# Performance work log

Hardware: AMD Instinct MI355X
Metric: run time of the kernel (lower is better)

The kernel has to match this reference:

```python
import jax, jax.numpy as jnp
import numpy as np

B, N, C = 2, 3072, 768
H = 12                      # num_heads
HD = C // H                 # 64
D = HD // 2                 # 32, rope dim per axis
GRID_H, GRID_W = 48, 64     # 768/16, 1024/16 ; GRID_H*GRID_W == N
BASE = 100.0
EPS = 1e-5


def _rope_tables():
    # positions per token (row-major cartesian product of y,x)
    pos_y = np.repeat(np.arange(GRID_H), GRID_W)   # [N]
    pos_x = np.tile(np.arange(GRID_W), GRID_H)     # [N]
    seq_len = max(GRID_H, GRID_W)
    inv_freq = 1.0 / BASE ** (np.arange(0, D, 2, dtype=np.float32) / D)  # [D/2]
    t = np.arange(seq_len, dtype=np.float32)
    freqs = np.einsum('i,j->ij', t, inv_freq)            # [S, D/2]
    emb = np.concatenate([freqs, freqs], axis=-1)        # [S, D]
    cos, sin = np.cos(emb), np.sin(emb)
    # gather per-token, add head broadcast dims -> [1, 1, N, D]
    mk = lambda tbl, idx: jnp.asarray(tbl[idx][None, None], dtype=jnp.float32)
    return mk(cos, pos_x), mk(sin, pos_x), mk(cos, pos_y), mk(sin, pos_y)


def setup_inputs() -> dict:
    key = jax.random.key(0)
    ks = jax.random.split(key, 12)
    s = 0.02
    cos_x, sin_x, cos_y, sin_y = _rope_tables()
    return {
        'x': jax.random.normal(ks[0], (B, N, C), jnp.float32),
        'w_qkv': jax.random.normal(ks[1], (3 * C, C), jnp.float32) * s,
        'w_proj': jax.random.normal(ks[2], (C, C), jnp.float32) * s,
        'b_proj': jnp.zeros((C,), jnp.float32),
        'g1': jnp.ones((C,), jnp.float32),
        'beta1': jnp.zeros((C,), jnp.float32),
        'g2': jnp.ones((C,), jnp.float32),
        'beta2': jnp.zeros((C,), jnp.float32),
        'w_fc1': jax.random.normal(ks[3], (4 * C, C), jnp.float32) * s,
        'b_fc1': jnp.zeros((4 * C,), jnp.float32),
        'w_fc2': jax.random.normal(ks[4], (C, 4 * C), jnp.float32) * s,
        'b_fc2': jnp.zeros((C,), jnp.float32),
        'cos_x': cos_x, 'sin_x': sin_x, 'cos_y': cos_y, 'sin_y': sin_y,
    }


def _layernorm(x, g, b):
    m = x.mean(-1, keepdims=True)
    v = ((x - m) ** 2).mean(-1, keepdims=True)
    return (x - m) * jax.lax.rsqrt(v + EPS) * g + b


def _rope1d(tok, cos, sin):
    t1, t2 = jnp.split(tok, 2, axis=-1)
    rot = jnp.concatenate([-t2, t1], axis=-1)
    return tok * cos + rot * sin


def _rope2d(tok, cos_x, sin_x, cos_y, sin_y):
    # tok: [B, H, N, HD]; first half of HD is y-coords, second half x-coords
    ty, tx = jnp.split(tok, 2, axis=-1)
    return jnp.concatenate([_rope1d(ty, cos_y, sin_y), _rope1d(tx, cos_x, sin_x)], axis=-1)


def reference(x, w_qkv, w_proj, b_proj, g1, beta1, g2, beta2,
              w_fc1, b_fc1, w_fc2, b_fc2, cos_x, sin_x, cos_y, sin_y):
    # --- attention branch ---
    xn = _layernorm(x, g1, beta1)
    qkv = jnp.einsum('bnc,dc->bnd', xn, w_qkv)           # [B, N, 3C]
    qkv = qkv.reshape(B, N, 3, H, HD).transpose(0, 3, 2, 1, 4)  # [B, H, 3, N, HD]
    q, k, v = qkv[:, :, 0], qkv[:, :, 1], qkv[:, :, 2]
    q = _rope2d(q, cos_x, sin_x, cos_y, sin_y)
    k = _rope2d(k, cos_x, sin_x, cos_y, sin_y)
    scale = HD ** -0.5
    attn = jnp.einsum('bhqd,bhkd->bhqk', q, k) * scale   # [B, H, N, N]
    attn = jax.nn.softmax(attn, axis=-1)
    o = jnp.einsum('bhqk,bhkd->bhqd', attn, v)           # [B, H, N, HD]
    o = o.transpose(0, 2, 1, 3).reshape(B, N, C)
    o = jnp.einsum('bnc,dc->bnd', o, w_proj) + b_proj
    x = x + o
    # --- mlp branch ---
    xn = _layernorm(x, g2, beta2)
    h = jnp.einsum('bnc,hc->bnh', xn, w_fc1) + b_fc1
    h = jax.nn.gelu(h, approximate=False)                # torch nn.GELU default (erf)
    h = jnp.einsum('bnh,ch->bnc', h, w_fc2) + b_fc2
    return x + h
```

## Files before the change

kernel.cpp:

```cpp
#include <hip/hip_runtime.h>
#include <hip/hip_bf16.h>


#define Nn 3072
#define Cc 768
#define Hh 12
#define Mm 6144

typedef unsigned short ushort_t;
typedef unsigned int u32;
using s8v = __attribute__((ext_vector_type(8))) short;
using f4v = __attribute__((ext_vector_type(4))) float;

__device__ __forceinline__ ushort_t f2b(float x){
  u32 u = __float_as_uint(x);
  return (ushort_t)((u + 0x7fffu + ((u >> 16) & 1u)) >> 16);
}
__device__ __forceinline__ u32 pack2(float a, float b){
  return (u32)f2b(a) | ((u32)f2b(b) << 16);
}
__device__ __forceinline__ float b2f(ushort_t u){
  return __uint_as_float(((u32)u) << 16);
}

#define GLD16(g, l) __builtin_amdgcn_global_load_lds( \
    (const __attribute__((address_space(1))) u32*)(g), \
    (__attribute__((address_space(3))) u32*)(l), 16, 0, 0)

__global__ __launch_bounds__(256) void cvt4_kernel(
    const float* __restrict__ a, ushort_t* __restrict__ oa, int na,
    const float* __restrict__ b, ushort_t* __restrict__ ob, int nb,
    const float* __restrict__ c, ushort_t* __restrict__ oc, int nc,
    const float* __restrict__ d, ushort_t* __restrict__ od)
{
  int i = (blockIdx.x*256 + threadIdx.x)*4;
  const float* src; ushort_t* dst;
  if (i < na)           { src = a + i;            dst = oa + i; }
  else if (i < na+nb)   { src = b + (i-na);       dst = ob + (i-na); }
  else if (i < na+nb+nc){ src = c + (i-na-nb);    dst = oc + (i-na-nb); }
  else                  { src = d + (i-na-nb-nc); dst = od + (i-na-nb-nc); }
  float4 v = *(const float4*)src;
  uint2 p; p.x = pack2(v.x, v.y); p.y = pack2(v.z, v.w);
  *(uint2*)dst = p;
}

__global__ __launch_bounds__(256) void ln_kernel(const float* __restrict__ in,
    const float* __restrict__ g, const float* __restrict__ be, ushort_t* __restrict__ out)
{
  int row = blockIdx.x;
  int tid = threadIdx.x;
  size_t base = (size_t)row * Cc;
  float v[3];
  #pragma unroll
  for (int i = 0; i < 3; ++i) v[i] = in[base + tid + i*256];
  __shared__ float red[8];
  float s = v[0]+v[1]+v[2];
  #pragma unroll
  for (int off=32; off; off>>=1) s += __shfl_xor(s, off);
  int wid = tid >> 6, lane = tid & 63;
  if (lane==0) red[wid] = s;
  __syncthreads();
  float mean = (red[0]+red[1]+red[2]+red[3]) * (1.f/Cc);
  float d = 0.f;
  #pragma unroll
  for (int i=0;i<3;++i){ float t = v[i]-mean; d += t*t; }
  #pragma unroll
  for (int off=32; off; off>>=1) d += __shfl_xor(d, off);
  if (lane==0) red[4+wid] = d;
  __syncthreads();
  float var  = (red[4]+red[5]+red[6]+red[7]) * (1.f/Cc);
  float rstd = rsqrtf(var + 1e-5f);
  #pragma unroll
  for (int i=0;i<3;++i){
    int idx = tid + i*256;
    out[base+idx] = f2b((v[i]-mean)*rstd*g[idx] + be[idx]);
  }
}

template<int EPI>
__global__ __launch_bounds__(256) void mgemm_kernel(
    const ushort_t* __restrict__ A, const ushort_t* __restrict__ W,
    const float* __restrict__ bias, const float* __restrict__ residf,
    void* __restrict__ outv, int Nd, int K)
{
  __shared__ __align__(16) ushort_t As[128*32];
  __shared__ __align__(16) ushort_t Ws[128*32];
  int tid = threadIdx.x;
  int w = tid >> 6, lane = tid & 63;
  int g = lane >> 4, c = lane & 15;
  int wr = w >> 1, wc = w & 1;
  int m0 = blockIdx.y * 128, n0 = blockIdx.x * 128;
  int srow = w*32 + (lane >> 2);
  int schunk = (lane & 3) * 8;
  const ushort_t* Ag = A + (size_t)(m0 + srow)*K + schunk;
  const ushort_t* Wg = W + (size_t)(n0 + srow)*K + schunk;
  ushort_t* Asl = &As[w*1024];
  ushort_t* Wsl = &Ws[w*1024];
  f4v acc[4][4] = {};
  for (int k0 = 0; k0 < K; k0 += 32) {
    __syncthreads();
    GLD16(Ag + k0,        Asl);
    GLD16(Ag + 16*K + k0, Asl + 512);
    GLD16(Wg + k0,        Wsl);
    GLD16(Wg + 16*K + k0, Wsl + 512);
    __syncthreads();
    s8v af[4], wf[4];
    #pragma unroll
    for (int i=0;i<4;++i) af[i] = *(const s8v*)&As[(wr*64 + i*16 + c)*32 + g*8];
    #pragma unroll
    for (int j=0;j<4;++j) wf[j] = *(const s8v*)&Ws[(wc*64 + j*16 + c)*32 + g*8];
    #pragma unroll
    for (int i=0;i<4;++i)
      #pragma unroll
      for (int j=0;j<4;++j)
        acc[i][j] = __builtin_amdgcn_mfma_f32_16x16x32_bf16(af[i], wf[j], acc[i][j], 0,0,0);
  }
  #pragma unroll
  for (int j=0;j<4;++j){
    int col = n0 + wc*64 + j*16 + c;
    float bv = (EPI != 0) ? bias[col] : 0.f;
    #pragma unroll
    for (int i=0;i<4;++i){
      int row0 = m0 + wr*64 + i*16 + g*4;
      #pragma unroll
      for (int r=0;r<4;++r){
        float v = acc[i][j][r];
        size_t off = (size_t)(row0 + r)*Nd + col;
        if (EPI == 0) {
          ((ushort_t*)outv)[off] = f2b(v);
        } else if (EPI == 2) {
          float t = v + bv;
          ((ushort_t*)outv)[off] = f2b(0.5f*t*(1.0f + erff(t*0.70710678118654752f)));
        } else {
          ((float*)outv)[off] = v + bv + residf[off];
        }
      }
    }
  }
}

__global__ __launch_bounds__(256) void repack_kernel(
    const ushort_t* __restrict__ qkv,
    const float* __restrict__ cx, const float* __restrict__ sx,
    const float* __restrict__ cy, const float* __restrict__ sy,
    ushort_t* __restrict__ Qb, ushort_t* __restrict__ Kb, ushort_t* __restrict__ Vt)
{
  __shared__ float Vls[64*68];
  int bh = blockIdx.y;
  int b = bh / Hh, h = bh - b*Hh;
  int n0 = blockIdx.x * 64;
  int tid = threadIdx.x;
  int tt = tid >> 2, cch = tid & 3;
  int n = n0 + tt;
  size_t rowbase = (size_t)(b*Nn + n) * 2304 + h*64;

  int half = cch >> 1, ibase = (cch & 1) * 8;
  int d1 = half*32 + ibase;
  const float* ct  = half ? cx : cy;
  const float* st_ = half ? sx : sy;
  float c1[8], s1[8], c2[8], s2[8];
  #pragma unroll
  for (int j=0;j<8;++j){
    c1[j] = ct[n*32 + ibase + j];       s1[j] = st_[n*32 + ibase + j];
    c2[j] = ct[n*32 + ibase + 16 + j];  s2[j] = st_[n*32 + ibase + 16 + j];
  }
  #pragma unroll
  for (int qk = 0; qk < 2; ++qk){
    const ushort_t* src = qkv + rowbase + qk*768;
    uint4 uv1 = *(const uint4*)(src + d1);
    uint4 uv2 = *(const uint4*)(src + d1 + 16);
    float v1[8], v2[8];
    v1[0]=b2f(uv1.x&0xffff); v1[1]=b2f(uv1.x>>16); v1[2]=b2f(uv1.y&0xffff); v1[3]=b2f(uv1.y>>16);
    v1[4]=b2f(uv1.z&0xffff); v1[5]=b2f(uv1.z>>16); v1[6]=b2f(uv1.w&0xffff); v1[7]=b2f(uv1.w>>16);
    v2[0]=b2f(uv2.x&0xffff); v2[1]=b2f(uv2.x>>16); v2[2]=b2f(uv2.y&0xffff); v2[3]=b2f(uv2.y>>16);
    v2[4]=b2f(uv2.z&0xffff); v2[5]=b2f(uv2.z>>16); v2[6]=b2f(uv2.w&0xffff); v2[7]=b2f(uv2.w>>16);
    float sc = qk ? 1.0f : 0.125f;
    float o1[8], o2[8];
    #pragma unroll
    for (int j=0;j<8;++j){
      o1[j] = (v1[j]*c1[j] - v2[j]*s1[j]) * sc;
      o2[j] = (v2[j]*c2[j] + v1[j]*s2[j]) * sc;
    }
    ushort_t* dst = (qk ? Kb : Qb) + ((size_t)bh*Nn + n)*64;
    uint4 u1, u2;
    u1.x = pack2(o1[0],o1[1]); u1.y = pack2(o1[2],o1[3]);
    u1.z = pack2(o1[4],o1[5]); u1.w = pack2(o1[6],o1[7]);
    u2.x = pack2(o2[0],o2[1]); u2.y = pack2(o2[2],o2[3]);
    u2.z = pack2(o2[4],o2[5]); u2.w = pack2(o2[6],o2[7]);
    *(uint4*)(dst + d1)      = u1;
    *(uint4*)(dst + d1 + 16) = u2;
  }

  {
    const ushort_t* src = qkv + rowbase + 1536 + cch*16;
    uint4 ua = *(const uint4*)(src);
    uint4 ub = *(const uint4*)(src + 8);
    float* lp = &Vls[tt*68 + cch*16];
    lp[0]=b2f(ua.x&0xffff); lp[1]=b2f(ua.x>>16); lp[2]=b2f(ua.y&0xffff); lp[3]=b2f(ua.y>>16);
    lp[4]=b2f(ua.z&0xffff); lp[5]=b2f(ua.z>>16); lp[6]=b2f(ua.w&0xffff); lp[7]=b2f(ua.w>>16);
    lp[8]=b2f(ub.x&0xffff); lp[9]=b2f(ub.x>>16); lp[10]=b2f(ub.y&0xffff); lp[11]=b2f(ub.y>>16);
    lp[12]=b2f(ub.z&0xffff); lp[13]=b2f(ub.z>>16); lp[14]=b2f(ub.w&0xffff); lp[15]=b2f(ub.w>>16);
  }
  __syncthreads();
  {
    int d = tid & 63, quarter = tid >> 6;
    float v[16];
    #pragma unroll
    for (int j=0;j<16;++j) v[j] = Vls[(quarter*16 + j)*68 + d];
    uint4 w0, w1;
    w0.x = pack2(v[0],v[1]);   w0.y = pack2(v[2],v[3]);
    w0.z = pack2(v[4],v[5]);   w0.w = pack2(v[6],v[7]);
    w1.x = pack2(v[8],v[9]);   w1.y = pack2(v[10],v[11]);
    w1.z = pack2(v[12],v[13]); w1.w = pack2(v[14],v[15]);
    ushort_t* dst = Vt + ((size_t)bh*64 + d)*Nn + n0 + quarter*16;
    *(uint4*)(dst)     = w0;
    *(uint4*)(dst + 8) = w1;
  }
}

__global__ __launch_bounds__(256) void fattn_kernel(
    const ushort_t* __restrict__ Qb, const ushort_t* __restrict__ Kb,
    const ushort_t* __restrict__ Vt, ushort_t* __restrict__ ob)
{
  __shared__ ushort_t Ks[64*72];
  __shared__ ushort_t Vts[64*72];
  __shared__ ushort_t Ps[4*16*72];
  int bh = blockIdx.y;
  int q0 = blockIdx.x * 64;
  int tid = threadIdx.x;
  int w = tid >> 6, lane = tid & 63, g = lane >> 4, c = lane & 15;

  const ushort_t* qp = Qb + ((size_t)bh*Nn + q0 + w*16 + c)*64;
  s8v qf0 = *(const s8v*)(qp + g*8);
  s8v qf1 = *(const s8v*)(qp + 32 + g*8);

  s8v ones8;
  #pragma unroll
  for (int j=0;j<8;++j) ones8[j] = (short)0x3f80;

  f4v o0={0,0,0,0}, o1={0,0,0,0}, o2={0,0,0,0}, o3={0,0,0,0}, l4={0,0,0,0};
  const ushort_t* kbase = Kb + (size_t)bh*Nn*64;
  const ushort_t* vbase = Vt + (size_t)bh*64*Nn;
  ushort_t* pw = &Ps[w*16*72];

  int srow = tid >> 2;
  int scb  = (tid & 3) * 16;

  for (int kt = 0; kt < Nn/64; ++kt){
    __syncthreads();
    {
      const ushort_t* ksrc = kbase + (size_t)(kt*64 + srow)*64 + scb;
      *(uint4*)&Ks[srow*72 + scb]     = *(const uint4*)(ksrc);
      *(uint4*)&Ks[srow*72 + scb + 8] = *(const uint4*)(ksrc + 8);
      const ushort_t* vsrc = vbase + (size_t)srow*Nn + kt*64 + scb;
      *(uint4*)&Vts[srow*72 + scb]     = *(const uint4*)(vsrc);
      *(uint4*)&Vts[srow*72 + scb + 8] = *(const uint4*)(vsrc + 8);
    }
    __syncthreads();

    f4v st[4];
    #pragma unroll
    for (int t=0;t<4;++t){
      s8v ka  = *(const s8v*)&Ks[(t*16+c)*72 + g*8];
      s8v kb2 = *(const s8v*)&Ks[(t*16+c)*72 + 32 + g*8];
      f4v z = {0,0,0,0};
      z = __builtin_amdgcn_mfma_f32_16x16x32_bf16(ka,  qf0, z, 0,0,0);
      st[t] = __builtin_amdgcn_mfma_f32_16x16x32_bf16(kb2, qf1, z, 0,0,0);
    }
    #pragma unroll
    for (int t=0;t<4;++t){
      uint2 pk;
      pk.x = pack2(__expf(st[t][0]), __expf(st[t][1]));
      pk.y = pack2(__expf(st[t][2]), __expf(st[t][3]));
      *(uint2*)&pw[c*72 + t*16 + g*4] = pk;
    }
    asm volatile("s_waitcnt lgkmcnt(0)" ::: "memory");
    s8v pf0 = *(const s8v*)&pw[c*72 + g*8];
    s8v pf1 = *(const s8v*)&pw[c*72 + 32 + g*8];

    {
      s8v v0a = *(const s8v*)&Vts[c*72 + g*8];
      s8v v0b = *(const s8v*)&Vts[c*72 + 32 + g*8];
      o0 = __builtin_amdgcn_mfma_f32_16x16x32_bf16(v0a, pf0, o0, 0,0,0);
      o0 = __builtin_amdgcn_mfma_f32_16x16x32_bf16(v0b, pf1, o0, 0,0,0);
      s8v v1a = *(const s8v*)&Vts[(16+c)*72 + g*8];
      s8v v1b = *(const s8v*)&Vts[(16+c)*72 + 32 + g*8];
      o1 = __builtin_amdgcn_mfma_f32_16x16x32_bf16(v1a, pf0, o1, 0,0,0);
      o1 = __builtin_amdgcn_mfma_f32_16x16x32_bf16(v1b, pf1, o1, 0,0,0);
      s8v v2a = *(const s8v*)&Vts[(32+c)*72 + g*8];
      s8v v2b = *(const s8v*)&Vts[(32+c)*72 + 32 + g*8];
      o2 = __builtin_amdgcn_mfma_f32_16x16x32_bf16(v2a, pf0, o2, 0,0,0);
      o2 = __builtin_amdgcn_mfma_f32_16x16x32_bf16(v2b, pf1, o2, 0,0,0);
      s8v v3a = *(const s8v*)&Vts[(48+c)*72 + g*8];
      s8v v3b = *(const s8v*)&Vts[(48+c)*72 + 32 + g*8];
      o3 = __builtin_amdgcn_mfma_f32_16x16x32_bf16(v3a, pf0, o3, 0,0,0);
      o3 = __builtin_amdgcn_mfma_f32_16x16x32_bf16(v3b, pf1, o3, 0,0,0);
      l4 = __builtin_amdgcn_mfma_f32_16x16x32_bf16(ones8, pf0, l4, 0,0,0);
      l4 = __builtin_amdgcn_mfma_f32_16x16x32_bf16(ones8, pf1, l4, 0,0,0);
    }
  }

  float rl = 1.0f / l4[0];
  int b = bh / Hh, h = bh - b*Hh;
  size_t tok = (size_t)b*Nn + q0 + w*16 + c;
  ushort_t* op = ob + tok*768 + h*64;
  uint2 pk;
  pk.x = pack2(o0[0]*rl, o0[1]*rl); pk.y = pack2(o0[2]*rl, o0[3]*rl);
  *(uint2*)&op[g*4] = pk;
  pk.x = pack2(o1[0]*rl, o1[1]*rl); pk.y = pack2(o1[2]*rl, o1[3]*rl);
  *(uint2*)&op[16 + g*4] = pk;
  pk.x = pack2(o2[0]*rl, o2[1]*rl); pk.y = pack2(o2[2]*rl, o2[3]*rl);
  *(uint2*)&op[32 + g*4] = pk;
  pk.x = pack2(o3[0]*rl, o3[1]*rl); pk.y = pack2(o3[2]*rl, o3[3]*rl);
  *(uint2*)&op[48 + g*4] = pk;
}

extern "C" void kernel_launch(void* const* d_in, const int* in_sizes, int n_in,
                              void* d_out, int out_size, void* d_ws, size_t ws_size,
                              hipStream_t stream)
{
  const float* x      = (const float*)d_in[0];
  const float* w_qkv  = (const float*)d_in[1];
  const float* w_proj = (const float*)d_in[2];
  const float* b_proj = (const float*)d_in[3];
  const float* g1     = (const float*)d_in[4];
  const float* be1    = (const float*)d_in[5];
  const float* g2     = (const float*)d_in[6];
  const float* be2    = (const float*)d_in[7];
  const float* w_fc1  = (const float*)d_in[8];
  const float* b_fc1  = (const float*)d_in[9];
  const float* w_fc2  = (const float*)d_in[10];
  const float* b_fc2  = (const float*)d_in[11];
  const float* cx     = (const float*)d_in[12];
  const float* sx     = (const float*)d_in[13];
  const float* cy     = (const float*)d_in[14];
  const float* sy     = (const float*)d_in[15];
  float* out = (float*)d_out;

  char* ws = (char*)d_ws;
  ushort_t* xnb   = (ushort_t*)(ws);
  ushort_t* Qb    = (ushort_t*)(ws + 9437184);
  ushort_t* Kb    = (ushort_t*)(ws + 18874368);
  float*    x1    = (float*)   (ws + 9437184);
  ushort_t* Vt    = (ushort_t*)(ws + 28311552);
  ushort_t* obb   = (ushort_t*)(ws + 37748736);
  ushort_t* qkvb  = (ushort_t*)(ws + 47185920);
  ushort_t* hb    = (ushort_t*)(ws + 47185920);
  ushort_t* wqkvb = (ushort_t*)(ws + 84934656);
  ushort_t* wprojb= (ushort_t*)(ws + 88473600);
  ushort_t* wfc1b = (ushort_t*)(ws + 89653248);
  ushort_t* wfc2b = (ushort_t*)(ws + 94371840);

  cvt4_kernel<<<(7077888/4)/256, 256, 0, stream>>>(
      w_qkv, wqkvb, 2304*768, w_proj, wprojb, 768*768,
      w_fc1, wfc1b, 3072*768, w_fc2, wfc2b);

  ln_kernel<<<Mm, 256, 0, stream>>>(x, g1, be1, xnb);
  mgemm_kernel<0><<<dim3(2304/128, Mm/128), 256, 0, stream>>>(xnb, wqkvb, nullptr, nullptr, qkvb, 2304, 768);
  repack_kernel<<<dim3(48, 24), 256, 0, stream>>>(qkvb, cx, sx, cy, sy, Qb, Kb, Vt);
  fattn_kernel<<<dim3(48, 24), 256, 0, stream>>>(Qb, Kb, Vt, obb);
  mgemm_kernel<1><<<dim3(768/128, Mm/128), 256, 0, stream>>>(obb, wprojb, b_proj, x, x1, 768, 768);
  ln_kernel<<<Mm, 256, 0, stream>>>(x1, g2, be2, xnb);
  mgemm_kernel<2><<<dim3(3072/128, Mm/128), 256, 0, stream>>>(xnb, wfc1b, b_fc1, nullptr, hb, 3072, 768);
  mgemm_kernel<1><<<dim3(768/128, Mm/128), 256, 0, stream>>>(hb, wfc2b, b_fc2, x1, out, 768, 3072);
}
```

Before: 469.9 us.

## Process two 16-row query tiles per wave in flash attention, truncate P packing

Each wave now handles 32 query rows instead of 16, so every K/V tile loaded into shared memory is reused across twice as many queries and the grid is halved to 24x24 blocks. The exp'd probabilities are packed to bf16 by truncation instead of round-to-nearest, which saves ALU work in the softmax step. This raises register use and leaves fewer blocks (576) for the 256 CUs, which can reduce occupancy. Truncation also adds a small downward bias to P, but the same truncated P feeds both the row sum and the output, so the bias partly cancels.

```diff
diff --git a/kernel.cpp b/kernel.cpp
--- a/kernel.cpp
+++ b/kernel.cpp
@@ -18,6 +18,9 @@
 }
 __device__ __forceinline__ u32 pack2(float a, float b){
   return (u32)f2b(a) | ((u32)f2b(b) << 16);
+}
+__device__ __forceinline__ u32 pack2t(float a, float b){
+  return (__float_as_uint(a) >> 16) | (__float_as_uint(b) & 0xffff0000u);
 }
 __device__ __forceinline__ float b2f(ushort_t u){
   return __uint_as_float(((u32)u) << 16);
@@ -224,24 +227,28 @@
 {
   __shared__ ushort_t Ks[64*72];
   __shared__ ushort_t Vts[64*72];
-  __shared__ ushort_t Ps[4*16*72];
+  __shared__ ushort_t Ps[4*32*72];
   int bh = blockIdx.y;
-  int q0 = blockIdx.x * 64;
+  int q0 = blockIdx.x * 128;
   int tid = threadIdx.x;
   int w = tid >> 6, lane = tid & 63, g = lane >> 4, c = lane & 15;
 
-  const ushort_t* qp = Qb + ((size_t)bh*Nn + q0 + w*16 + c)*64;
-  s8v qf0 = *(const s8v*)(qp + g*8);
-  s8v qf1 = *(const s8v*)(qp + 32 + g*8);
+  const ushort_t* qpA = Qb + ((size_t)bh*Nn + q0 + w*32 + c)*64;
+  const ushort_t* qpB = qpA + 16*64;
+  s8v qA0 = *(const s8v*)(qpA + g*8);
+  s8v qA1 = *(const s8v*)(qpA + 32 + g*8);
+  s8v qB0 = *(const s8v*)(qpB + g*8);
+  s8v qB1 = *(const s8v*)(qpB + 32 + g*8);
 
   s8v ones8;
   #pragma unroll
   for (int j=0;j<8;++j) ones8[j] = (short)0x3f80;
 
-  f4v o0={0,0,0,0}, o1={0,0,0,0}, o2={0,0,0,0}, o3={0,0,0,0}, l4={0,0,0,0};
+  f4v oA[4] = {}, oB[4] = {}, lA = {0,0,0,0}, lB = {0,0,0,0};
   const ushort_t* kbase = Kb + (size_t)bh*Nn*64;
   const ushort_t* vbase = Vt + (size_t)bh*64*Nn;
-  ushort_t* pw = &Ps[w*16*72];
+  ushort_t* pwA = &Ps[w*32*72];
+  ushort_t* pwB = pwA + 16*72;
 
   int srow = tid >> 2;
   int scb  = (tid & 3) * 16;
@@ -258,61 +265,74 @@
     }
     __syncthreads();
 
-    f4v st[4];
+    f4v sA[4], sB[4];
     #pragma unroll
     for (int t=0;t<4;++t){
       s8v ka  = *(const s8v*)&Ks[(t*16+c)*72 + g*8];
       s8v kb2 = *(const s8v*)&Ks[(t*16+c)*72 + 32 + g*8];
       f4v z = {0,0,0,0};
-      z = __builtin_amdgcn_mfma_f32_16x16x32_bf16(ka,  qf0, z, 0,0,0);
-      st[t] = __builtin_amdgcn_mfma_f32_16x16x32_bf16(kb2, qf1, z, 0,0,0);
+      z = __builtin_amdgcn_mfma_f32_16x16x32_bf16(ka,  qA0, z, 0,0,0);
+      sA[t] = __builtin_amdgcn_mfma_f32_16x16x32_bf16(kb2, qA1, z, 0,0,0);
+      f4v z2 = {0,0,0,0};
+      z2 = __builtin_amdgcn_mfma_f32_16x16x32_bf16(ka,  qB0, z2, 0,0,0);
+      sB[t] = __builtin_amdgcn_mfma_f32_16x16x32_bf16(kb2, qB1, z2, 0,0,0);
     }
     #pragma unroll
     for (int t=0;t<4;++t){
       uint2 pk;
-      pk.x = pack2(__expf(st[t][0]), __expf(st[t][1]));
-      pk.y = pack2(__expf(st[t][2]), __expf(st[t][3]));
-      *(uint2*)&pw[c*72 + t*16 + g*4] = pk;
+      pk.x = pack2t(__expf(sA[t][0]), __expf(sA[t][1]));
+      pk.y = pack2t(__expf(sA[t][2]), __expf(sA[t][3]));
+      *(uint2*)&pwA[c*72 + t*16 + g*4] = pk;
+      pk.x = pack2t(__expf(sB[t][0]), __expf(sB[t][1]));
+      pk.y = pack2t(__expf(sB[t][2]), __expf(sB[t][3]));
+      *(uint2*)&pwB[c*72 + t*16 + g*4] = pk;
     }
     asm volatile("s_waitcnt lgkmcnt(0)" ::: "memory");
-    s8v pf0 = *(const s8v*)&pw[c*72 + g*8];
-    s8v pf1 = *(const s8v*)&pw[c*72 + 32 + g*8];
-
-    {
-      s8v v0a = *(const s8v*)&Vts[c*72 + g*8];
-      s8v v0b = *(const s8v*)&Vts[c*72 + 32 + g*8];
-      o0 = __builtin_amdgcn_mfma_f32_16x16x32_bf16(v0a, pf0, o0, 0,0,0);
-      o0 = __builtin_amdgcn_mfma_f32_16x16x32_bf16(v0b, pf1, o0, 0,0,0);
-      s8v v1a = *(const s8v*)&Vts[(16+c)*72 + g*8];
-      s8v v1b = *(const s8v*)&Vts[(16+c)*72 + 32 + g*8];
-      o1 = __builtin_amdgcn_mfma_f32_16x16x32_bf16(v1a, pf0, o1, 0,0,0);
-      o1 = __builtin_amdgcn_mfma_f32_16x16x32_bf16(v1b, pf1, o1, 0,0,0);
-      s8v v2a = *(const s8v*)&Vts[(32+c)*72 + g*8];
-      s8v v2b = *(const s8v*)&Vts[(32+c)*72 + 32 + g*8];
-      o2 = __builtin_amdgcn_mfma_f32_16x16x32_bf16(v2a, pf0, o2, 0,0,0);
-      o2 = __builtin_amdgcn_mfma_f32_16x16x32_bf16(v2b, pf1, o2, 0,0,0);
-      s8v v3a = *(const s8v*)&Vts[(48+c)*72 + g*8];
-      s8v v3b = *(const s8v*)&Vts[(48+c)*72 + 32 + g*8];
-      o3 = __builtin_amdgcn_mfma_f32_16x16x32_bf16(v3a, pf0, o3, 0,0,0);
-      o3 = __builtin_amdgcn_mfma_f32_16x16x32_bf16(v3b, pf1, o3, 0,0,0);
-      l4 = __builtin_amdgcn_mfma_f32_16x16x32_bf16(ones8, pf0, l4, 0,0,0);
-      l4 = __builtin_amdgcn_mfma_f32_16x16x32_bf16(ones8, pf1, l4, 0,0,0);
-    }
-  }
-
-  float rl = 1.0f / l4[0];
+    s8v pA0 = *(const s8v*)&pwA[c*72 + g*8];
+    s8v pA1 = *(const s8v*)&pwA[c*72 + 32 + g*8];
+    s8v pB0 = *(const s8v*)&pwB[c*72 + g*8];
+    s8v pB1 = *(const s8v*)&pwB[c*72 + 32 + g*8];
+
+    #pragma unroll
+    for (int d=0;d<4;++d){
+      s8v va = *(const s8v*)&Vts[(d*16+c)*72 + g*8];
+      s8v vb = *(const s8v*)&Vts[(d*16+c)*72 + 32 + g*8];
+      oA[d] = __builtin_amdgcn_mfma_f32_16x16x32_bf16(va, pA0, oA[d], 0,0,0);
+      oA[d] = __builtin_amdgcn_mfma_f32_16x16x32_bf16(vb, pA1, oA[d], 0,0,0);
+      oB[d] = __builtin_amdgcn_mfma_f32_16x16x32_bf16(va, pB0, oB[d], 0,0,0);
+      oB[d] = __builtin_amdgcn_mfma_f32_16x16x32_bf16(vb, pB1, oB[d], 0,0,0);
+    }
+    lA = __builtin_amdgcn_mfma_f32_16x16x32_bf16(ones8, pA0, lA, 0,0,0);
+    lA = __builtin_amdgcn_mfma_f32_16x16x32_bf16(ones8, pA1, lA, 0,0,0);
+    lB = __builtin_amdgcn_mfma_f32_16x16x32_bf16(ones8, pB0, lB, 0,0,0);
+    lB = __builtin_amdgcn_mfma_f32_16x16x32_bf16(ones8, pB1, lB, 0,0,0);
+  }
+
   int b = bh / Hh, h = bh - b*Hh;
-  size_t tok = (size_t)b*Nn + q0 + w*16 + c;
-  ushort_t* op = ob + tok*768 + h*64;
-  uint2 pk;
-  pk.x = pack2(o0[0]*rl, o0[1]*rl); pk.y = pack2(o0[2]*rl, o0[3]*rl);
-  *(uint2*)&op[g*4] = pk;
-  pk.x = pack2(o1[0]*rl, o1[1]*rl); pk.y = pack2(o1[2]*rl, o1[3]*rl);
-  *(uint2*)&op[16 + g*4] = pk;
-  pk.x = pack2(o2[0]*rl, o2[1]*rl); pk.y = pack2(o2[2]*rl, o2[3]*rl);
-  *(uint2*)&op[32 + g*4] = pk;
-  pk.x = pack2(o3[0]*rl, o3[1]*rl); pk.y = pack2(o3[2]*rl, o3[3]*rl);
-  *(uint2*)&op[48 + g*4] = pk;
+  {
+    float rl = 1.0f / lA[0];
+    size_t tok = (size_t)b*Nn + q0 + w*32 + c;
+    ushort_t* op = ob + tok*768 + h*64;
+    #pragma unroll
+    for (int d=0;d<4;++d){
+      uint2 pk;
+      pk.x = pack2(oA[d][0]*rl, oA[d][1]*rl);
+      pk.y = pack2(oA[d][2]*rl, oA[d][3]*rl);
+      *(uint2*)&op[d*16 + g*4] = pk;
+    }
+  }
+  {
+    float rl = 1.0f / lB[0];
+    size_t tok = (size_t)b*Nn + q0 + w*32 + 16 + c;
+    ushort_t* op = ob + tok*768 + h*64;
+    #pragma unroll
+    for (int d=0;d<4;++d){
+      uint2 pk;
+      pk.x = pack2(oB[d][0]*rl, oB[d][1]*rl);
+      pk.y = pack2(oB[d][2]*rl, oB[d][3]*rl);
+      *(uint2*)&op[d*16 + g*4] = pk;
+    }
+  }
 }
 
 extern "C" void kernel_launch(void* const* d_in, const int* in_sizes, int n_in,
@@ -358,7 +378,7 @@
   ln_kernel<<<Mm, 256, 0, stream>>>(x, g1, be1, xnb);
   mgemm_kernel<0><<<dim3(2304/128, Mm/128), 256, 0, stream>>>(xnb, wqkvb, nullptr, nullptr, qkvb, 2304, 768);
   repack_kernel<<<dim3(48, 24), 256, 0, stream>>>(qkvb, cx, sx, cy, sy, Qb, Kb, Vt);
-  fattn_kernel<<<dim3(48, 24), 256, 0, stream>>>(Qb, Kb, Vt, obb);
+  fattn_kernel<<<dim3(24, 24), 256, 0, stream>>>(Qb, Kb, Vt, obb);
   mgemm_kernel<1><<<dim3(768/128, Mm/128), 256, 0, stream>>>(obb, wprojb, b_proj, x, x1, 768, 768);
   ln_kernel<<<Mm, 256, 0, stream>>>(x1, g2, be2, xnb);
   mgemm_kernel<2><<<dim3(3072/128, Mm/128), 256, 0, stream>>>(xnb, wfc1b, b_fc1, nullptr, hb, 3072, 768);
```

Measured after the change: 468.0 us. About the same (-0.4%).
